# Optimization experiments

Measured on AMD Instinct MI355X. Metric: run time of the kernel, lower is better.

The kernel has to match this reference:

```python
import jax, jax.numpy as jnp
import numpy as np

NUM_CLASSES = 21
NEGPOS_RATIO = 3
B, P = 64, 24564


def setup_inputs() -> dict:
    key = jax.random.key(0)
    ks = jax.random.split(key, 10)
    return {
        "loc_data": jax.random.normal(ks[0], (B, P, 4), jnp.float32),
        "conf_data": jax.random.normal(ks[1], (B, P, NUM_CLASSES), jnp.float32),
        "has_lp_data": jax.random.normal(ks[2], (B, P, 2), jnp.float32),
        "size_lp_data": jax.random.normal(ks[3], (B, P, 2), jnp.float32),
        "offset_data": jax.random.normal(ks[4], (B, P, 2), jnp.float32),
        "loc_t": jax.random.normal(ks[5], (B, P, 4), jnp.float32),
        "conf_t": jax.random.randint(ks[6], (B, P), 0, NUM_CLASSES, jnp.int64),
        "has_lp_t": jax.random.randint(ks[7], (B, P), 0, 2, jnp.int64),
        "size_lp_t": jax.random.normal(ks[8], (B, P, 2), jnp.float32),
        "offset_t": jax.random.normal(ks[9], (B, P, 2), jnp.float32),
    }


def _smooth_l1_sum(p, t, mask):
    # sum-reduced smooth L1 (beta=1) over elements selected by mask
    d = jnp.abs(p - t)
    l = jnp.where(d < 1.0, 0.5 * d * d, d - 0.5)
    return jnp.sum(l * mask)


def _ce_per_row(logits, labels):
    # per-row cross entropy: logsumexp(logits) - logits[label]
    lse = jax.nn.logsumexp(logits, axis=-1)
    g = jnp.take_along_axis(logits, labels[..., None], axis=-1)[..., 0]
    return lse - g


def reference(loc_data, conf_data, has_lp_data, size_lp_data, offset_data,
              loc_t, conf_t, has_lp_t, size_lp_t, offset_t):
    dt = loc_data.dtype
    num_priors = conf_data.shape[1]
    pos = conf_t > 0                                  # [B,P]
    posf = pos.astype(dt)[..., None]                  # [B,P,1]

    # localization loss over positives
    loss_l = _smooth_l1_sum(loc_data, loc_t, posf)

    # size / offset losses over positives, gated by has_lp flag
    hlp = has_lp_t.astype(dt)[..., None]              # [B,P,1]
    loss_size_lp = _smooth_l1_sum(size_lp_data * hlp, size_lp_t * hlp, posf)
    loss_offset = _smooth_l1_sum(offset_data * hlp, offset_t * hlp, posf)

    # hard negative mining on per-prior conf CE
    ce = _ce_per_row(conf_data, conf_t)               # [B,P]
    ce_mine = jnp.where(pos, 0.0, ce)
    loss_idx = jnp.argsort(-ce_mine, axis=1)          # descending sort indices
    idx_rank = jnp.argsort(loss_idx, axis=1)          # rank of each prior
    num_pos = jnp.sum(pos, axis=1, keepdims=True)     # [B,1]
    num_neg = jnp.clip(NEGPOS_RATIO * num_pos, None, num_priors - 1)
    neg = idx_rank < num_neg                          # [B,P]
    sel = (pos | neg).astype(dt)

    loss_c = jnp.sum(ce * sel)
    loss_has_lp = jnp.sum(_ce_per_row(has_lp_data, has_lp_t) * sel)

    N = jnp.sum(pos).astype(dt)
    return (loss_l / N, loss_c / N, loss_size_lp / N,
            loss_offset / N, loss_has_lp / N)
```

## Files before the change

### kernel.cpp

```cpp
#include <hip/hip_runtime.h>
#include <stdint.h>

#define NC 21
#define BATCH 64
#define PRI 24564
#define NROWS (BATCH * PRI)
#define SLABS 32
#define SLABR 768
#define GBLK (BATCH * SLABS)
#define SENT 0xFFFFFFFFu

typedef float f4a4 __attribute__((ext_vector_type(4), aligned(4)));

__device__ __forceinline__ float sl1f(float p, float t) {
    float d = fabsf(p - t);
    return d < 1.0f ? 0.5f * d * d : d - 0.5f;
}

__device__ __forceinline__ unsigned int f2k(float v) {
    unsigned int u = __float_as_uint(v);
    return (u & 0x80000000u) ? ~u : (u | 0x80000000u);
}

__device__ __forceinline__ unsigned int chkey(float2 ch) {
    unsigned hb = __float_as_uint(ch.y);
    return (hb & 0x80000000u) ? 0x80000000u : f2k(ch.x);
}

__device__ __forceinline__ double blockReduce(double v, double* sred) {
    #pragma unroll
    for (int off = 32; off > 0; off >>= 1)
        v += __shfl_down(v, off, 64);
    const int wid = threadIdx.x >> 6, lane = threadIdx.x & 63;
    __syncthreads();
    if (lane == 0) sred[wid] = v;
    __syncthreads();
    double r = 0.0;
    if (threadIdx.x == 0) r = sred[0] + sred[1] + sred[2] + sred[3];
    return r;
}

__global__ __launch_bounds__(256, 4) void k_main(
    const float* __restrict__ loc_data, const float* __restrict__ conf_data,
    const float* __restrict__ has_lp_data, const float* __restrict__ size_lp_data,
    const float* __restrict__ offset_data, const float* __restrict__ loc_t,
    const int* __restrict__ conf_t, const int* __restrict__ has_lp_t,
    const float* __restrict__ size_lp_t, const float* __restrict__ offset_t,
    float2* __restrict__ ws_ch, int* __restrict__ numpos, double* __restrict__ part,
    int* __restrict__ ghist1)
{
    __shared__ int hist[4096];
    __shared__ double sred[4];
    const int tid = threadIdx.x;
    const int b = blockIdx.x >> 5, s = blockIdx.x & 31;
    for (int k = tid; k < 4096; k += 256) hist[k] = 0;
    __syncthreads();

    int pr[3]; bool vld[3];
    #pragma unroll
    for (int i = 0; i < 3; ++i) {
        int p = s * SLABR + i * 256 + tid;
        vld[i] = p < PRI;
        pr[i] = vld[i] ? p : PRI - 1;
    }
    const unsigned rb = (unsigned)b * PRI;

    int ct[3];
    #pragma unroll
    for (int i = 0; i < 3; ++i) ct[i] = conf_t[rb + pr[i]];
    f4a4 cw[3][5]; float c20[3], gg[3];
    #pragma unroll
    for (int i = 0; i < 3; ++i) {
        const float* crow = conf_data + (long)(rb + pr[i]) * NC;
        #pragma unroll
        for (int j = 0; j < 5; ++j) cw[i][j] = ((const f4a4*)crow)[j];
        c20[i] = crow[20];
        gg[i] = crow[ct[i]];
    }
    float ce[3];
    #pragma unroll
    for (int i = 0; i < 3; ++i) {
        float m = c20[i];
        #pragma unroll
        for (int j = 0; j < 5; ++j)
            m = fmaxf(m, fmaxf(fmaxf(cw[i][j].x, cw[i][j].y), fmaxf(cw[i][j].z, cw[i][j].w)));
        float sum = __expf(c20[i] - m);
        #pragma unroll
        for (int j = 0; j < 5; ++j)
            sum += __expf(cw[i][j].x - m) + __expf(cw[i][j].y - m)
                 + __expf(cw[i][j].z - m) + __expf(cw[i][j].w - m);
        ce[i] = m + __logf(sum) - gg[i];
    }
    #pragma unroll
    for (int i = 0; i < 3; ++i) {
        if (vld[i] && ct[i] <= 0) {
            unsigned key = f2k(ce[i]);
            if (key != 0x80000000u) atomicAdd(&hist[key >> 20], 1);
        }
    }

    int hl[3]; float4 lp[3], lt[3]; float2 sp2[3], st2[3], op2[3], ot2[3], hh[3];
    #pragma unroll
    for (int i = 0; i < 3; ++i) {
        const unsigned r = rb + pr[i];
        hl[i] = has_lp_t[r];
        lp[i] = ((const float4*)loc_data)[r];
        lt[i] = ((const float4*)loc_t)[r];
        sp2[i] = ((const float2*)size_lp_data)[r];
        st2[i] = ((const float2*)size_lp_t)[r];
        op2[i] = ((const float2*)offset_data)[r];
        ot2[i] = ((const float2*)offset_t)[r];
        hh[i] = ((const float2*)has_lp_data)[r];
    }
    double aL = 0.0, aS = 0.0, aO = 0.0;
    int myp = 0;
    #pragma unroll
    for (int i = 0; i < 3; ++i) {
        const bool pos = ct[i] > 0;
        float ll = sl1f(lp[i].x, lt[i].x) + sl1f(lp[i].y, lt[i].y)
                 + sl1f(lp[i].z, lt[i].z) + sl1f(lp[i].w, lt[i].w);
        float ls = sl1f(sp2[i].x, st2[i].x) + sl1f(sp2[i].y, st2[i].y);
        float lo = sl1f(op2[i].x, ot2[i].x) + sl1f(op2[i].y, ot2[i].y);
        const float pf = (vld[i] && pos) ? 1.f : 0.f;
        const float hf = (hl[i] != 0) ? 1.f : 0.f;
        aL += (double)(pf * ll);
        aS += (double)(pf * hf * ls);
        aO += (double)(pf * hf * lo);
        float hm = fmaxf(hh[i].x, hh[i].y);
        float hs = __expf(hh[i].x - hm) + __expf(hh[i].y - hm);
        float hlce = fmaxf(hm + __logf(hs) - (hl[i] != 0 ? hh[i].y : hh[i].x), 0.0f);
        unsigned hb = __float_as_uint(hlce) | (pos ? 0x80000000u : 0u);
        if (vld[i]) ws_ch[rb + pr[i]] = make_float2(ce[i], __uint_as_float(hb));
        myp += (vld[i] && pos) ? 1 : 0;
    }

    double v;
    v = blockReduce(aL, sred); if (tid == 0) part[0 * GBLK + blockIdx.x] = v;
    v = blockReduce(aS, sred); if (tid == 0) part[1 * GBLK + blockIdx.x] = v;
    v = blockReduce(aO, sred); if (tid == 0) part[2 * GBLK + blockIdx.x] = v;
    v = blockReduce((double)myp, sred);
    if (tid == 0 && v > 0.0) atomicAdd(&numpos[b], (int)(v + 0.5));

    __syncthreads();
    for (int k = tid; k < 4096; k += 256) {
        int h = hist[k];
        if (h) atomicAdd(&ghist1[(b << 12) + k], h);
    }
}

__global__ __launch_bounds__(256) void k_pick0(
    const int* __restrict__ ghist1, const int* __restrict__ numpos,
    unsigned* __restrict__ prefix_io, int* __restrict__ rem_io,
    unsigned* __restrict__ selT, int* __restrict__ needed)
{
    const int b = blockIdx.x, tid = threadIdx.x;
    __shared__ int sct[256];
    __shared__ unsigned s_dig;
    __shared__ int s_rem;

    int K = 3 * numpos[b]; if (K > PRI - 1) K = PRI - 1;

    int h[16];
    const int* g = ghist1 + (b << 12) + tid * 16;
    int ctn = 0;
    #pragma unroll
    for (int j = 0; j < 16; ++j) { h[j] = g[j]; ctn += h[j]; }
    sct[tid] = ctn;
    __syncthreads();
    #pragma unroll
    for (int off = 1; off < 256; off <<= 1) {
        int v = (tid + off < 256) ? sct[tid + off] : 0;
        __syncthreads();
        sct[tid] += v;
        __syncthreads();
    }
    const int M = sct[0];

    if (K <= 0) {
        if (tid == 0) { selT[b] = 0xFFFFFFFFu; needed[b] = 0; rem_io[b] = 0; prefix_io[b] = SENT; }
        return;
    }
    if (K > M) {
        if (tid == 0) { selT[b] = 0x80000000u; needed[b] = K - M; rem_io[b] = 0; prefix_io[b] = SENT; }
        return;
    }
    const int Safter = (tid < 255) ? sct[tid + 1] : 0;
    int cum = Safter;
    #pragma unroll
    for (int j = 15; j >= 0; --j) {
        int c2 = cum + h[j];
        if (c2 >= K && cum < K) { s_dig = (unsigned)(tid * 16 + j); s_rem = K - cum; }
        cum = c2;
    }
    __syncthreads();
    if (tid == 0) { prefix_io[b] = s_dig; rem_io[b] = s_rem; }
}

template<int MSHIFT, int BSHIFT>
__global__ __launch_bounds__(256) void k_hist(
    const float2* __restrict__ ws_ch, const unsigned* __restrict__ prefix_io,
    int* __restrict__ ghist)
{
    const int b = blockIdx.x >> 5, s = blockIdx.x & 31;
    const unsigned pref = prefix_io[b];
    if (pref == SENT) return;
    __shared__ int hist[1024];
    const int tid = threadIdx.x;
    for (int k = tid; k < 1024; k += 256) hist[k] = 0;
    __syncthreads();
    #pragma unroll
    for (int i = 0; i < 3; ++i) {
        const int p = s * SLABR + i * 256 + tid;
        if (p < PRI) {
            unsigned key = chkey(ws_ch[(unsigned)b * PRI + p]);
            if (key != 0x80000000u && (key >> MSHIFT) == pref)
                atomicAdd(&hist[(key >> BSHIFT) & 1023], 1);
        }
    }
    __syncthreads();
    for (int k = tid; k < 1024; k += 256) {
        int h = hist[k];
        if (h) atomicAdd(&ghist[(b << 10) + k], h);
    }
}

template<int ROUND>
__global__ __launch_bounds__(256) void k_pickR(
    const int* __restrict__ ghist, unsigned* __restrict__ prefix_io,
    int* __restrict__ rem_io, unsigned* __restrict__ selT, int* __restrict__ needed)
{
    const int b = blockIdx.x, tid = threadIdx.x;
    const int rem = rem_io[b];
    if (rem <= 0) return;
    __shared__ int sct[256];
    __shared__ unsigned s_dig;
    __shared__ int s_rem;
    int h[4];
    const int* g = ghist + (b << 10) + tid * 4;
    int ctn = 0;
    #pragma unroll
    for (int j = 0; j < 4; ++j) { h[j] = g[j]; ctn += h[j]; }
    sct[tid] = ctn;
    __syncthreads();
    #pragma unroll
    for (int off = 1; off < 256; off <<= 1) {
        int v = (tid + off < 256) ? sct[tid + off] : 0;
        __syncthreads();
        sct[tid] += v;
        __syncthreads();
    }
    const int Safter = (tid < 255) ? sct[tid + 1] : 0;
    int cum = Safter;
    #pragma unroll
    for (int j = 3; j >= 0; --j) {
        int c2 = cum + h[j];
        if (c2 >= rem && cum < rem) { s_dig = (unsigned)(tid * 4 + j); s_rem = rem - cum; }
        cum = c2;
    }
    __syncthreads();
    if (tid == 0) {
        if (ROUND == 1) { prefix_io[b] = (prefix_io[b] << 10) | s_dig; rem_io[b] = s_rem; }
        else            { selT[b] = (prefix_io[b] << 10) | s_dig;      needed[b] = s_rem; }
    }
}

__global__ __launch_bounds__(256) void k_sel2(
    const float2* __restrict__ ws_ch, const unsigned* __restrict__ selT,
    int* __restrict__ cntT, double* __restrict__ sums)
{
    __shared__ double sred[4];
    const int tid = threadIdx.x;
    const int b = blockIdx.x >> 5, s = blockIdx.x & 31;
    const unsigned T = selT[b];
    double aC = 0.0, aH = 0.0, tC = 0.0, tH = 0.0, cc = 0.0;
    #pragma unroll
    for (int i = 0; i < 3; ++i) {
        const int p = s * SLABR + i * 256 + tid;
        if (p < PRI) {
            float2 ch = ws_ch[(unsigned)b * PRI + p];
            unsigned hb = __float_as_uint(ch.y);
            const bool pos = (hb >> 31) != 0;
            const unsigned key = pos ? 0x80000000u : f2k(ch.x);
            const float hlv = __uint_as_float(hb & 0x7fffffffu);
            if (pos || key > T) { aC += (double)ch.x; aH += (double)hlv; }
            if (key == T) {
                cc += 1.0;
                if (!pos) { tC += (double)ch.x; tH += (double)hlv; }
            }
        }
    }
    double v;
    v = blockReduce(aC, sred); if (tid == 0) sums[0 * GBLK + blockIdx.x] = v;
    v = blockReduce(aH, sred); if (tid == 0) sums[1 * GBLK + blockIdx.x] = v;
    v = blockReduce(tC, sred); if (tid == 0) sums[2 * GBLK + blockIdx.x] = v;
    v = blockReduce(tH, sred); if (tid == 0) sums[3 * GBLK + blockIdx.x] = v;
    v = blockReduce(cc, sred); if (tid == 0) cntT[blockIdx.x] = (int)(v + 0.5);
}

__global__ __launch_bounds__(256) void k_cut(
    const float2* __restrict__ ws_ch, const unsigned* __restrict__ selT,
    const int* __restrict__ needed, const int* __restrict__ cntT,
    const double* __restrict__ sums, double* __restrict__ lossCH)
{
    const int b = blockIdx.x, tid = threadIdx.x;
    __shared__ double sred[4];
    __shared__ int scnt_s[32];
    __shared__ int s_sl, s_loc, s_found;
    __shared__ int wtot[4];
    const int need = needed[b];
    const unsigned T = selT[b];

    if (tid < 32) scnt_s[tid] = cntT[b * 32 + tid];
    __syncthreads();
    if (tid == 0) {
        int sl = 32, loc = 0, cum = 0;
        if (need > 0) {
            for (int s2 = 0; s2 < 32; ++s2) {
                int c2 = scnt_s[s2];
                if (cum + c2 >= need) { sl = s2; loc = need - cum; break; }
                cum += c2;
            }
        }
        s_sl = sl; s_loc = loc; s_found = -1;
    }
    __syncthreads();
    const int sl = s_sl, loc = s_loc;

    double aC = 0.0, aH = 0.0;
    if (tid < 32) {
        aC = sums[0 * GBLK + b * 32 + tid] + (tid < sl ? sums[2 * GBLK + b * 32 + tid] : 0.0);
        aH = sums[1 * GBLK + b * 32 + tid] + (tid < sl ? sums[3 * GBLK + b * 32 + tid] : 0.0);
    }
    double totC = blockReduce(aC, sred);
    double totH = blockReduce(aH, sred);

    if (sl < 32) {
        int run = 0;
        for (int i = 0; i < 3; ++i) {
            const int p = sl * SLABR + i * 256 + tid;
            bool eq = false;
            if (p < PRI) eq = (chkey(ws_ch[(unsigned)b * PRI + p]) == T);
            const unsigned long long m = __ballot(eq);
            const int lane = tid & 63, wid = tid >> 6;
            if (lane == 0) wtot[wid] = __popcll(m);
            const int mex = __popcll(m & ((1ull << lane) - 1ull));
            __syncthreads();
            int woff = 0;
            for (int w = 0; w < wid; ++w) woff += wtot[w];
            if (eq && (run + woff + mex + 1 == loc)) s_found = p;
            __syncthreads();
            run += wtot[0] + wtot[1] + wtot[2] + wtot[3];
            __syncthreads();
        }
        const int cutoff = s_found;
        double pC = 0.0, pH = 0.0;
        for (int i = 0; i < 3; ++i) {
            const int p = sl * SLABR + i * 256 + tid;
            if (p < PRI && p <= cutoff) {
                float2 ch = ws_ch[(unsigned)b * PRI + p];
                unsigned hb = __float_as_uint(ch.y);
                const bool pos = (hb >> 31) != 0;
                const unsigned key = pos ? 0x80000000u : f2k(ch.x);
                if (!pos && key == T) {
                    pC += (double)ch.x;
                    pH += (double)__uint_as_float(hb & 0x7fffffffu);
                }
            }
        }
        double v1 = blockReduce(pC, sred);
        double v2 = blockReduce(pH, sred);
        if (tid == 0) { totC += v1; totH += v2; }
    }
    if (tid == 0) { lossCH[b] = totC; lossCH[64 + b] = totH; }
}

__global__ __launch_bounds__(256) void k_final(
    const double* __restrict__ part, const int* __restrict__ numpos,
    const double* __restrict__ lossCH, float* __restrict__ out)
{
    __shared__ double sred[4];
    const int tid = threadIdx.x;
    double s[3];
    #pragma unroll
    for (int k = 0; k < 3; ++k) {
        double a = 0.0;
        for (int t = tid; t < GBLK; t += 256) a += part[k * GBLK + t];
        s[k] = blockReduce(a, sred);
    }
    double lc = (tid < BATCH) ? lossCH[tid] : 0.0;
    lc = blockReduce(lc, sred);
    double lh = (tid < BATCH) ? lossCH[64 + tid] : 0.0;
    lh = blockReduce(lh, sred);
    double n = (tid < BATCH) ? (double)numpos[tid] : 0.0;
    n = blockReduce(n, sred);
    if (tid == 0) {
        out[0] = (float)(s[0] / n);
        out[1] = (float)(lc / n);
        out[2] = (float)(s[1] / n);
        out[3] = (float)(s[2] / n);
        out[4] = (float)(lh / n);
    }
}

extern "C" void kernel_launch(void* const* d_in, const int* in_sizes, int n_in,
                              void* d_out, int out_size, void* d_ws, size_t ws_size,
                              hipStream_t stream)
{
    const float* loc_data     = (const float*)d_in[0];
    const float* conf_data    = (const float*)d_in[1];
    const float* has_lp_data  = (const float*)d_in[2];
    const float* size_lp_data = (const float*)d_in[3];
    const float* offset_data  = (const float*)d_in[4];
    const float* loc_t        = (const float*)d_in[5];
    const int*   conf_t       = (const int*)d_in[6];
    const int*   has_lp_t     = (const int*)d_in[7];
    const float* size_lp_t    = (const float*)d_in[8];
    const float* offset_t     = (const float*)d_in[9];
    float* out = (float*)d_out;

    char* ws = (char*)d_ws;
    int* numpos      = (int*)(ws + 0);
    unsigned* selT   = (unsigned*)(ws + 256);
    int* needed      = (int*)(ws + 512);
    unsigned* prefix = (unsigned*)(ws + 768);
    int* rem         = (int*)(ws + 1024);
    int* cntT        = (int*)(ws + 1536);
    double* part     = (double*)(ws + 16384);
    double* sums     = (double*)(ws + 65536);
    double* lossCH   = (double*)(ws + 131072);
    int* ghist1      = (int*)(ws + 132096);
    int* ghist2      = (int*)(ws + 1180672);
    int* ghist3      = (int*)(ws + 1442816);
    float2* ws_ch    = (float2*)(ws + 1704960);

    hipMemsetAsync(ws, 0, 256, stream);
    hipMemsetAsync(ws + 132096, 0, 1572864, stream);

    k_main<<<GBLK, 256, 0, stream>>>(loc_data, conf_data, has_lp_data, size_lp_data,
                                     offset_data, loc_t, conf_t, has_lp_t,
                                     size_lp_t, offset_t, ws_ch, numpos, part, ghist1);
    k_pick0<<<BATCH, 256, 0, stream>>>(ghist1, numpos, prefix, rem, selT, needed);
    k_hist<20, 10><<<GBLK, 256, 0, stream>>>(ws_ch, prefix, ghist2);
    k_pickR<1><<<BATCH, 256, 0, stream>>>(ghist2, prefix, rem, selT, needed);
    k_hist<10, 0><<<GBLK, 256, 0, stream>>>(ws_ch, prefix, ghist3);
    k_pickR<2><<<BATCH, 256, 0, stream>>>(ghist3, prefix, rem, selT, needed);
    k_sel2<<<GBLK, 256, 0, stream>>>(ws_ch, selT, cntT, sums);
    k_cut<<<BATCH, 256, 0, stream>>>(ws_ch, selT, needed, cntT, sums, lossCH);
    k_final<<<1, 256, 0, stream>>>(part, numpos, lossCH, out);
}
```

Before: 334.3 us.

## Split main kernel into CE and small-loss kernels with separate CE/hl arrays

Splits the fused main kernel into a conf-CE kernel that builds the histogram and a separate kernel for the localization, size and offset losses. The packed float2 (ce, hl) workspace becomes two float arrays, so the radix-select passes read only the 4-byte keys. CE is now computed without max-subtraction, which removes a pass but risks overflow for large logits. The change adds a launch and re-reads conf_t.

```diff
diff --git a/kernel.cpp b/kernel.cpp
--- a/kernel.cpp
+++ b/kernel.cpp
@@ -17,14 +17,15 @@
     return d < 1.0f ? 0.5f * d * d : d - 0.5f;
 }
 
-__device__ __forceinline__ unsigned int f2k(float v) {
-    unsigned int u = __float_as_uint(v);
-    return (u & 0x80000000u) ? ~u : (u | 0x80000000u);
-}
-
-__device__ __forceinline__ unsigned int chkey(float2 ch) {
-    unsigned hb = __float_as_uint(ch.y);
-    return (hb & 0x80000000u) ? 0x80000000u : f2k(ch.x);
+__device__ __forceinline__ unsigned kdec(float v, bool* pos, float* ce) {
+    unsigned u = __float_as_uint(v);
+    *pos = (u >> 31) != 0;
+    *ce = __uint_as_float(u & 0x7fffffffu);
+    return *pos ? 0x80000000u : (u | 0x80000000u);
+}
+__device__ __forceinline__ unsigned kdec_key(float v) {
+    unsigned u = __float_as_uint(v);
+    return (u >> 31) ? 0x80000000u : (u | 0x80000000u);
 }
 
 __device__ __forceinline__ double blockReduce(double v, double* sred) {
@@ -40,21 +41,73 @@
     return r;
 }
 
-__global__ __launch_bounds__(256, 4) void k_main(
-    const float* __restrict__ loc_data, const float* __restrict__ conf_data,
-    const float* __restrict__ has_lp_data, const float* __restrict__ size_lp_data,
-    const float* __restrict__ offset_data, const float* __restrict__ loc_t,
-    const int* __restrict__ conf_t, const int* __restrict__ has_lp_t,
-    const float* __restrict__ size_lp_t, const float* __restrict__ offset_t,
-    float2* __restrict__ ws_ch, int* __restrict__ numpos, double* __restrict__ part,
-    int* __restrict__ ghist1)
+__global__ __launch_bounds__(256) void k_ce(
+    const float* __restrict__ conf_data, const int* __restrict__ conf_t,
+    float* __restrict__ ws_ce, int* __restrict__ ghist1)
 {
     __shared__ int hist[4096];
+    const int tid = threadIdx.x;
+    const int b = blockIdx.x >> 5, s = blockIdx.x & 31;
+    for (int k = tid; k < 4096; k += 256) hist[k] = 0;
+    __syncthreads();
+    const unsigned rb = (unsigned)b * PRI;
+
+    int pr[3]; bool vld[3]; int ct[3];
+    #pragma unroll
+    for (int i = 0; i < 3; ++i) {
+        int p = s * SLABR + i * 256 + tid;
+        vld[i] = p < PRI;
+        pr[i] = vld[i] ? p : PRI - 1;
+        ct[i] = conf_t[rb + pr[i]];
+    }
+
+    #pragma unroll
+    for (int i = 0; i < 3; ++i) {
+        const int c = ct[i];
+        const float* crow = conf_data + (long)(rb + pr[i]) * NC;
+        float sum = 0.f, g = 0.f;
+        #pragma unroll
+        for (int j = 0; j < 5; ++j) {
+            f4a4 v = ((const f4a4*)crow)[j];
+            sum += __expf(v.x) + __expf(v.y) + __expf(v.z) + __expf(v.w);
+            g = (4*j+0 == c) ? v.x : g;
+            g = (4*j+1 == c) ? v.y : g;
+            g = (4*j+2 == c) ? v.z : g;
+            g = (4*j+3 == c) ? v.w : g;
+        }
+        float x20 = crow[20];
+        sum += __expf(x20);
+        g = (20 == c) ? x20 : g;
+        float ce = fmaxf(__logf(sum) - g, 0.0f);
+        const bool pos = c > 0;
+        unsigned u = __float_as_uint(ce) | (pos ? 0x80000000u : 0u);
+        if (vld[i]) {
+            ws_ce[rb + pr[i]] = __uint_as_float(u);
+            if (!pos) {
+                unsigned key = __float_as_uint(ce) | 0x80000000u;
+                if (key != 0x80000000u) atomicAdd(&hist[key >> 20], 1);
+            }
+        }
+    }
+    __syncthreads();
+    for (int k = tid; k < 4096; k += 256) {
+        int h = hist[k];
+        if (h) atomicAdd(&ghist1[(b << 12) + k], h);
+    }
+}
+
+__global__ __launch_bounds__(256) void k_small(
+    const float* __restrict__ loc_data, const float* __restrict__ has_lp_data,
+    const float* __restrict__ size_lp_data, const float* __restrict__ offset_data,
+    const float* __restrict__ loc_t, const int* __restrict__ conf_t,
+    const int* __restrict__ has_lp_t, const float* __restrict__ size_lp_t,
+    const float* __restrict__ offset_t,
+    float* __restrict__ ws_hl, int* __restrict__ numpos, double* __restrict__ part)
+{
     __shared__ double sred[4];
     const int tid = threadIdx.x;
     const int b = blockIdx.x >> 5, s = blockIdx.x & 31;
-    for (int k = tid; k < 4096; k += 256) hist[k] = 0;
-    __syncthreads();
+    const unsigned rb = (unsigned)b * PRI;
 
     int pr[3]; bool vld[3];
     #pragma unroll
@@ -63,89 +116,42 @@
         vld[i] = p < PRI;
         pr[i] = vld[i] ? p : PRI - 1;
     }
-    const unsigned rb = (unsigned)b * PRI;
-
-    int ct[3];
-    #pragma unroll
-    for (int i = 0; i < 3; ++i) ct[i] = conf_t[rb + pr[i]];
-    f4a4 cw[3][5]; float c20[3], gg[3];
-    #pragma unroll
-    for (int i = 0; i < 3; ++i) {
-        const float* crow = conf_data + (long)(rb + pr[i]) * NC;
-        #pragma unroll
-        for (int j = 0; j < 5; ++j) cw[i][j] = ((const f4a4*)crow)[j];
-        c20[i] = crow[20];
-        gg[i] = crow[ct[i]];
-    }
-    float ce[3];
-    #pragma unroll
-    for (int i = 0; i < 3; ++i) {
-        float m = c20[i];
-        #pragma unroll
-        for (int j = 0; j < 5; ++j)
-            m = fmaxf(m, fmaxf(fmaxf(cw[i][j].x, cw[i][j].y), fmaxf(cw[i][j].z, cw[i][j].w)));
-        float sum = __expf(c20[i] - m);
-        #pragma unroll
-        for (int j = 0; j < 5; ++j)
-            sum += __expf(cw[i][j].x - m) + __expf(cw[i][j].y - m)
-                 + __expf(cw[i][j].z - m) + __expf(cw[i][j].w - m);
-        ce[i] = m + __logf(sum) - gg[i];
-    }
-    #pragma unroll
-    for (int i = 0; i < 3; ++i) {
-        if (vld[i] && ct[i] <= 0) {
-            unsigned key = f2k(ce[i]);
-            if (key != 0x80000000u) atomicAdd(&hist[key >> 20], 1);
-        }
-    }
-
-    int hl[3]; float4 lp[3], lt[3]; float2 sp2[3], st2[3], op2[3], ot2[3], hh[3];
-    #pragma unroll
-    for (int i = 0; i < 3; ++i) {
-        const unsigned r = rb + pr[i];
-        hl[i] = has_lp_t[r];
-        lp[i] = ((const float4*)loc_data)[r];
-        lt[i] = ((const float4*)loc_t)[r];
-        sp2[i] = ((const float2*)size_lp_data)[r];
-        st2[i] = ((const float2*)size_lp_t)[r];
-        op2[i] = ((const float2*)offset_data)[r];
-        ot2[i] = ((const float2*)offset_t)[r];
-        hh[i] = ((const float2*)has_lp_data)[r];
-    }
+
     double aL = 0.0, aS = 0.0, aO = 0.0;
     int myp = 0;
     #pragma unroll
     for (int i = 0; i < 3; ++i) {
-        const bool pos = ct[i] > 0;
-        float ll = sl1f(lp[i].x, lt[i].x) + sl1f(lp[i].y, lt[i].y)
-                 + sl1f(lp[i].z, lt[i].z) + sl1f(lp[i].w, lt[i].w);
-        float ls = sl1f(sp2[i].x, st2[i].x) + sl1f(sp2[i].y, st2[i].y);
-        float lo = sl1f(op2[i].x, ot2[i].x) + sl1f(op2[i].y, ot2[i].y);
+        const unsigned r = rb + pr[i];
+        const int c = conf_t[r];
+        const int hl = has_lp_t[r];
+        float4 lp = ((const float4*)loc_data)[r];
+        float4 lt = ((const float4*)loc_t)[r];
+        float2 sp = ((const float2*)size_lp_data)[r];
+        float2 st = ((const float2*)size_lp_t)[r];
+        float2 op = ((const float2*)offset_data)[r];
+        float2 ot = ((const float2*)offset_t)[r];
+        float2 hh = ((const float2*)has_lp_data)[r];
+        const bool pos = c > 0;
+        float ll = sl1f(lp.x, lt.x) + sl1f(lp.y, lt.y) + sl1f(lp.z, lt.z) + sl1f(lp.w, lt.w);
+        float ls = sl1f(sp.x, st.x) + sl1f(sp.y, st.y);
+        float lo = sl1f(op.x, ot.x) + sl1f(op.y, ot.y);
         const float pf = (vld[i] && pos) ? 1.f : 0.f;
-        const float hf = (hl[i] != 0) ? 1.f : 0.f;
+        const float hf = (hl != 0) ? 1.f : 0.f;
         aL += (double)(pf * ll);
         aS += (double)(pf * hf * ls);
         aO += (double)(pf * hf * lo);
-        float hm = fmaxf(hh[i].x, hh[i].y);
-        float hs = __expf(hh[i].x - hm) + __expf(hh[i].y - hm);
-        float hlce = fmaxf(hm + __logf(hs) - (hl[i] != 0 ? hh[i].y : hh[i].x), 0.0f);
-        unsigned hb = __float_as_uint(hlce) | (pos ? 0x80000000u : 0u);
-        if (vld[i]) ws_ch[rb + pr[i]] = make_float2(ce[i], __uint_as_float(hb));
+        float hm = fmaxf(hh.x, hh.y);
+        float hs = __expf(hh.x - hm) + __expf(hh.y - hm);
+        float hlce = fmaxf(hm + __logf(hs) - (hl != 0 ? hh.y : hh.x), 0.0f);
+        if (vld[i]) ws_hl[r] = hlce;
         myp += (vld[i] && pos) ? 1 : 0;
     }
-
     double v;
     v = blockReduce(aL, sred); if (tid == 0) part[0 * GBLK + blockIdx.x] = v;
     v = blockReduce(aS, sred); if (tid == 0) part[1 * GBLK + blockIdx.x] = v;
     v = blockReduce(aO, sred); if (tid == 0) part[2 * GBLK + blockIdx.x] = v;
     v = blockReduce((double)myp, sred);
     if (tid == 0 && v > 0.0) atomicAdd(&numpos[b], (int)(v + 0.5));
-
-    __syncthreads();
-    for (int k = tid; k < 4096; k += 256) {
-        int h = hist[k];
-        if (h) atomicAdd(&ghist1[(b << 12) + k], h);
-    }
 }
 
 __global__ __launch_bounds__(256) void k_pick0(
@@ -198,7 +204,7 @@
 
 template<int MSHIFT, int BSHIFT>
 __global__ __launch_bounds__(256) void k_hist(
-    const float2* __restrict__ ws_ch, const unsigned* __restrict__ prefix_io,
+    const float* __restrict__ ws_ce, const unsigned* __restrict__ prefix_io,
     int* __restrict__ ghist)
 {
     const int b = blockIdx.x >> 5, s = blockIdx.x & 31;
@@ -212,7 +218,7 @@
     for (int i = 0; i < 3; ++i) {
         const int p = s * SLABR + i * 256 + tid;
         if (p < PRI) {
-            unsigned key = chkey(ws_ch[(unsigned)b * PRI + p]);
+            unsigned key = kdec_key(ws_ce[(unsigned)b * PRI + p]);
             if (key != 0x80000000u && (key >> MSHIFT) == pref)
                 atomicAdd(&hist[(key >> BSHIFT) & 1023], 1);
         }
@@ -265,8 +271,9 @@
 }
 
 __global__ __launch_bounds__(256) void k_sel2(
-    const float2* __restrict__ ws_ch, const unsigned* __restrict__ selT,
-    int* __restrict__ cntT, double* __restrict__ sums)
+    const float* __restrict__ ws_ce, const float* __restrict__ ws_hl,
+    const unsigned* __restrict__ selT, int* __restrict__ cntT,
+    double* __restrict__ sums)
 {
     __shared__ double sred[4];
     const int tid = threadIdx.x;
@@ -277,15 +284,14 @@
     for (int i = 0; i < 3; ++i) {
         const int p = s * SLABR + i * 256 + tid;
         if (p < PRI) {
-            float2 ch = ws_ch[(unsigned)b * PRI + p];
-            unsigned hb = __float_as_uint(ch.y);
-            const bool pos = (hb >> 31) != 0;
-            const unsigned key = pos ? 0x80000000u : f2k(ch.x);
-            const float hlv = __uint_as_float(hb & 0x7fffffffu);
-            if (pos || key > T) { aC += (double)ch.x; aH += (double)hlv; }
+            const unsigned r = (unsigned)b * PRI + p;
+            bool pos; float ce;
+            const unsigned key = kdec(ws_ce[r], &pos, &ce);
+            const float hlv = ws_hl[r];
+            if (pos || key > T) { aC += (double)ce; aH += (double)hlv; }
             if (key == T) {
                 cc += 1.0;
-                if (!pos) { tC += (double)ch.x; tH += (double)hlv; }
+                if (!pos) { tC += (double)ce; tH += (double)hlv; }
             }
         }
     }
@@ -298,9 +304,10 @@
 }
 
 __global__ __launch_bounds__(256) void k_cut(
-    const float2* __restrict__ ws_ch, const unsigned* __restrict__ selT,
-    const int* __restrict__ needed, const int* __restrict__ cntT,
-    const double* __restrict__ sums, double* __restrict__ lossCH)
+    const float* __restrict__ ws_ce, const float* __restrict__ ws_hl,
+    const unsigned* __restrict__ selT, const int* __restrict__ needed,
+    const int* __restrict__ cntT, const double* __restrict__ sums,
+    double* __restrict__ lossCH)
 {
     const int b = blockIdx.x, tid = threadIdx.x;
     __shared__ double sred[4];
@@ -339,7 +346,7 @@
         for (int i = 0; i < 3; ++i) {
             const int p = sl * SLABR + i * 256 + tid;
             bool eq = false;
-            if (p < PRI) eq = (chkey(ws_ch[(unsigned)b * PRI + p]) == T);
+            if (p < PRI) eq = (kdec_key(ws_ce[(unsigned)b * PRI + p]) == T);
             const unsigned long long m = __ballot(eq);
             const int lane = tid & 63, wid = tid >> 6;
             if (lane == 0) wtot[wid] = __popcll(m);
@@ -357,13 +364,12 @@
         for (int i = 0; i < 3; ++i) {
             const int p = sl * SLABR + i * 256 + tid;
             if (p < PRI && p <= cutoff) {
-                float2 ch = ws_ch[(unsigned)b * PRI + p];
-                unsigned hb = __float_as_uint(ch.y);
-                const bool pos = (hb >> 31) != 0;
-                const unsigned key = pos ? 0x80000000u : f2k(ch.x);
+                const unsigned r = (unsigned)b * PRI + p;
+                bool pos; float ce;
+                const unsigned key = kdec(ws_ce[r], &pos, &ce);
                 if (!pos && key == T) {
-                    pC += (double)ch.x;
-                    pH += (double)__uint_as_float(hb & 0x7fffffffu);
+                    pC += (double)ce;
+                    pH += (double)ws_hl[r];
                 }
             }
         }
@@ -431,20 +437,22 @@
     int* ghist1      = (int*)(ws + 132096);
     int* ghist2      = (int*)(ws + 1180672);
     int* ghist3      = (int*)(ws + 1442816);
-    float2* ws_ch    = (float2*)(ws + 1704960);
+    float* ws_ce     = (float*)(ws + 1704960);
+    float* ws_hl     = (float*)(ws + 7993344);
 
     hipMemsetAsync(ws, 0, 256, stream);
     hipMemsetAsync(ws + 132096, 0, 1572864, stream);
 
-    k_main<<<GBLK, 256, 0, stream>>>(loc_data, conf_data, has_lp_data, size_lp_data,
-                                     offset_data, loc_t, conf_t, has_lp_t,
-                                     size_lp_t, offset_t, ws_ch, numpos, part, ghist1);
+    k_ce<<<GBLK, 256, 0, stream>>>(conf_data, conf_t, ws_ce, ghist1);
+    k_small<<<GBLK, 256, 0, stream>>>(loc_data, has_lp_data, size_lp_data, offset_data,
+                                      loc_t, conf_t, has_lp_t, size_lp_t, offset_t,
+                                      ws_hl, numpos, part);
     k_pick0<<<BATCH, 256, 0, stream>>>(ghist1, numpos, prefix, rem, selT, needed);
-    k_hist<20, 10><<<GBLK, 256, 0, stream>>>(ws_ch, prefix, ghist2);
+    k_hist<20, 10><<<GBLK, 256, 0, stream>>>(ws_ce, prefix, ghist2);
     k_pickR<1><<<BATCH, 256, 0, stream>>>(ghist2, prefix, rem, selT, needed);
-    k_hist<10, 0><<<GBLK, 256, 0, stream>>>(ws_ch, prefix, ghist3);
+    k_hist<10, 0><<<GBLK, 256, 0, stream>>>(ws_ce, prefix, ghist3);
     k_pickR<2><<<BATCH, 256, 0, stream>>>(ghist3, prefix, rem, selT, needed);
-    k_sel2<<<GBLK, 256, 0, stream>>>(ws_ch, selT, cntT, sums);
-    k_cut<<<BATCH, 256, 0, stream>>>(ws_ch, selT, needed, cntT, sums, lossCH);
+    k_sel2<<<GBLK, 256, 0, stream>>>(ws_ce, ws_hl, selT, cntT, sums);
+    k_cut<<<BATCH, 256, 0, stream>>>(ws_ce, ws_hl, selT, needed, cntT, sums, lossCH);
     k_final<<<1, 256, 0, stream>>>(part, numpos, lossCH, out);
 }
```

Result: no change. 335.8 us (+0.5%).
